# Performance work log

Measured on AMD Instinct MI355X. Metric: run time of the kernel, lower is better.

## Reference

```python
import jax, jax.numpy as jnp
import numpy as np

EPS = 1e-5
B, C, T = 128, 64, 1000          # batch, EEG channels, time samples
NCLU, HID, NOUT = 8, 512, 4      # clusters, head hidden dim, outputs (=feature_dim)


def _conv1d(x, w):
    # x: (N, Cin, T), w: (Cout, Cin, K), valid conv along time
    return jax.lax.conv_general_dilated(x, w, (1,), 'VALID',
                                        dimension_numbers=('NCH', 'OIH', 'NCH'))


def _bn(x, g, b, m, v):
    # eval-mode BatchNorm over channel dim of (N, C, T)
    return (x - m[None, :, None]) * (g / jnp.sqrt(v + EPS))[None, :, None] + b[None, :, None]


def _pool3(x):
    # maxpool kernel 3 stride 3 along time
    return jax.lax.reduce_window(x, -jnp.inf, jax.lax.max, (1, 1, 3), (1, 1, 3), 'VALID')


def setup_inputs() -> dict:
    key = jax.random.key(0)
    ks = jax.random.split(key, 12)
    def nrm(k, shape, fan):
        return jax.random.normal(k, shape, jnp.float32) / np.float32(np.sqrt(fan))
    inp = {
        'x': jax.random.normal(ks[0], (B, C, T), jnp.float32),
        'cluster_ids': jax.random.randint(ks[1], (B,), 0, NCLU, jnp.int32),
        # Deep4Net-style backbone params
        'w_time': nrm(ks[2], (25, 1, 10), 10),
        'b_time': jnp.zeros((25,), jnp.float32),
        'w_spat': nrm(ks[3], (25, 25, C), 25 * C),
        'w2': nrm(ks[4], (50, 25, 10), 250),
        'w3': nrm(ks[5], (100, 50, 10), 500),
        'w4': nrm(ks[6], (200, 100, 10), 1000),
        'w_cls': nrm(ks[7], (NOUT, 200, 7), 1400),
        'b_cls': jnp.zeros((NOUT,), jnp.float32),
        # per-cluster expert head params
        'hW1': nrm(ks[8], (NCLU, HID, NOUT), NOUT),
        'hb1': jnp.zeros((NCLU, HID), jnp.float32),
        'hW2': nrm(ks[9], (NCLU, NOUT, HID), HID),
        'hb2': jnp.zeros((NCLU, NOUT), jnp.float32),
        'hg': jnp.ones((NCLU, HID), jnp.float32),
        'hbe': jnp.zeros((NCLU, HID), jnp.float32),
        'hm': jnp.zeros((NCLU, HID), jnp.float32),
        'hv': jnp.ones((NCLU, HID), jnp.float32),
    }
    for i, c in zip((1, 2, 3, 4), (25, 50, 100, 200)):
        inp[f'g{i}'] = jnp.ones((c,), jnp.float32)
        inp[f'be{i}'] = jnp.zeros((c,), jnp.float32)
        inp[f'm{i}'] = jnp.zeros((c,), jnp.float32)
        inp[f'v{i}'] = jnp.ones((c,), jnp.float32)
    return inp


def reference(x, cluster_ids, w_time, b_time, w_spat, w2, w3, w4, w_cls, b_cls,
              hW1, hb1, hW2, hb2, hg, hbe, hm, hv,
              g1, be1, m1, v1, g2, be2, m2, v2, g3, be3, m3, v3, g4, be4, m4, v4):
    b_, c_, t_ = x.shape
    # conv_time: same 25 temporal filters applied per EEG channel -> (B, C, 25, T1)
    h = _conv1d(x.reshape(b_ * c_, 1, t_), w_time) + b_time[None, :, None]
    h = h.reshape(b_, c_, 25, -1)
    # conv_spat: collapse EEG channel axis -> (B, 25, T1)
    z = jnp.einsum('bcft,gfc->bgt', h, w_spat)
    z = _pool3(jax.nn.elu(_bn(z, g1, be1, m1, v1)))
    for w, g, be, m, v in ((w2, g2, be2, m2, v2), (w3, g3, be3, m3, v3), (w4, g4, be4, m4, v4)):
        z = _pool3(jax.nn.elu(_bn(_conv1d(z, w), g, be, m, v)))
    # final_conv_length='auto': classifier conv reduces time dim to 1 -> (B, NOUT)
    feats = (_conv1d(z, w_cls) + b_cls[None, :, None])[:, :, 0]
    # per-sample expert head routing (Linear -> BN(eval) -> ReLU -> [Dropout eval] -> Linear)
    h1 = jnp.einsum('bf,bhf->bh', feats, hW1[cluster_ids]) + hb1[cluster_ids]
    h1 = (h1 - hm[cluster_ids]) * (hg[cluster_ids] / jnp.sqrt(hv[cluster_ids] + EPS)) + hbe[cluster_ids]
    h1 = jax.nn.relu(h1)
    return jnp.einsum('bh,boh->bo', h1, hW2[cluster_ids]) + hb2[cluster_ids]
```

## Files before the change

### kernel.cpp

```cpp
#include <hip/hip_runtime.h>
#include <math.h>

#define EPS_BN 1e-5f

typedef __attribute__((ext_vector_type(8))) short short8;
typedef __attribute__((ext_vector_type(4))) float f32x4;
typedef __attribute__((ext_vector_type(4))) unsigned int uint4v;

__device__ __forceinline__ unsigned short f2bf(float f) {
    unsigned int u = __float_as_uint(f);
    u = (u + 0x7fffu + ((u >> 16) & 1u)) >> 16;
    return (unsigned short)u;
}
__device__ __forceinline__ float bf2f(unsigned short s) {
    return __uint_as_float(((unsigned int)s) << 16);
}
__device__ __forceinline__ float elu1(float y) { return y > 0.f ? y : expm1f(y); }
__device__ __forceinline__ float warp_sum(float v) {
    for (int off = 32; off > 0; off >>= 1) v += __shfl_down(v, off);
    return v;
}

#define UW1 0
#define UW2 20480
#define UW3 40960
#define UW4 122880
#define BB1 0
#define BB2 32
#define BB3 96
#define BB4 224
#define XTG_U 410496
#define Z1G_U 9192320
#define Z2G_U 10544000

#define NPREP 1602
#define RS_ZB 36

__global__ __launch_bounds__(256) void kprep_tr(
    const float* __restrict__ x,
    const float* __restrict__ w_time, const float* __restrict__ b_time,
    const float* __restrict__ w_spat,
    const float* __restrict__ w2, const float* __restrict__ w3,
    const float* __restrict__ w4,
    const float* __restrict__ g1, const float* __restrict__ be1,
    const float* __restrict__ m1, const float* __restrict__ v1,
    const float* __restrict__ g2, const float* __restrict__ be2,
    const float* __restrict__ m2, const float* __restrict__ v2,
    const float* __restrict__ g3, const float* __restrict__ be3,
    const float* __restrict__ m3, const float* __restrict__ v3,
    const float* __restrict__ g4, const float* __restrict__ be4,
    const float* __restrict__ m4, const float* __restrict__ v4,
    unsigned short* __restrict__ wsz, float* __restrict__ biasf) {
    __shared__ float tr[64 * 65];
    if (blockIdx.x < NPREP) {
        int idx = blockIdx.x * 256 + threadIdx.x;
        if (idx < 20480) {
            int k = idx >> 11, g = (idx >> 6) & 31, c = idx & 63;
            float val = 0.f;
            if (g < 25) {
                float s = 0.f;
#pragma unroll
                for (int f = 0; f < 25; ++f)
                    s = fmaf(w_spat[g * 1600 + f * 64 + c], w_time[f * 10 + k], s);
                val = s * (g1[g] * rsqrtf(v1[g] + EPS_BN));
            }
            wsz[UW1 + idx] = f2bf(val);
        } else if (idx < 40960) {
            int j = idx - 20480;
            int k = j >> 11, g = (j >> 5) & 63, c = j & 31;
            float val = 0.f;
            if (g < 50 && c < 25)
                val = w2[(g * 25 + c) * 10 + k] * (g2[g] * rsqrtf(v2[g] + EPS_BN));
            wsz[UW2 + j] = f2bf(val);
        } else if (idx < 122880) {
            int j = idx - 40960;
            int k = j >> 13, g = (j >> 6) & 127, c = j & 63;
            float val = 0.f;
            if (g < 100 && c < 50)
                val = w3[(g * 50 + c) * 10 + k] * (g3[g] * rsqrtf(v3[g] + EPS_BN));
            wsz[UW3 + j] = f2bf(val);
        } else if (idx < 409600) {
            int j = idx - 122880;
            int k = j / 28672, r = j % 28672, g = r >> 7, c = r & 127;
            float val = 0.f;
            if (g < 200 && c < 100)
                val = w4[(g * 100 + c) * 10 + k] * (g4[g] * rsqrtf(v4[g] + EPS_BN));
            wsz[UW4 + j] = f2bf(val);
        } else if (idx < 410048) {
            int j = idx - 409600;
            if (j < 32) {
                int g = j; float val = 0.f;
                if (g < 25) {
                    float beff = 0.f;
                    for (int f = 0; f < 25; ++f) {
                        float a = 0.f;
                        for (int c = 0; c < 64; ++c) a += w_spat[g * 1600 + f * 64 + c];
                        beff = fmaf(a, b_time[f], beff);
                    }
                    float sc = g1[g] * rsqrtf(v1[g] + EPS_BN);
                    val = be1[g] - m1[g] * sc + beff * sc;
                }
                biasf[BB1 + g] = val;
            } else if (j < 96) {
                int g = j - 32; float val = 0.f;
                if (g < 50) { float sc = g2[g] * rsqrtf(v2[g] + EPS_BN); val = be2[g] - m2[g] * sc; }
                biasf[BB2 + g] = val;
            } else if (j < 224) {
                int g = j - 96; float val = 0.f;
                if (g < 100) { float sc = g3[g] * rsqrtf(v3[g] + EPS_BN); val = be3[g] - m3[g] * sc; }
                biasf[BB3 + g] = val;
            } else {
                int g = j - 224; float val = 0.f;
                if (g < 200) { float sc = g4[g] * rsqrtf(v4[g] + EPS_BN); val = be4[g] - m4[g] * sc; }
                biasf[BB4 + g] = val;
            }
        }
    } else {
        const int bid = blockIdx.x - NPREP;
        const int b = bid / 17, tile = bid % 17, t = threadIdx.x;
        const int t0 = tile * 64;
        const float* xb = x + b * 64000;
        for (int idx = t; idx < 1024; idx += 256) {
            int c = idx >> 4, q = idx & 15;
            int tg = t0 + 4 * q;
            float4 v = {0.f, 0.f, 0.f, 0.f};
            if (tg + 4 <= 1000) {
                v = *(const float4*)(xb + c * 1000 + tg);
            } else {
                float* pv = (float*)&v;
#pragma unroll
                for (int e = 0; e < 4; ++e)
                    if (tg + e < 1000) pv[e] = xb[c * 1000 + tg + e];
            }
            tr[c * 65 + 4 * q]     = v.x;
            tr[c * 65 + 4 * q + 1] = v.y;
            tr[c * 65 + 4 * q + 2] = v.z;
            tr[c * 65 + 4 * q + 3] = v.w;
        }
        __syncthreads();
        unsigned short* xTg = wsz + XTG_U;
        for (int idx = t; idx < 2048; idx += 256) {
            int tl = idx >> 5, cp = idx & 31;
            int tg = t0 + tl;
            unsigned int pk = 0u;
            if (tg < 1000)
                pk = (unsigned int)f2bf(tr[(2 * cp) * 65 + tl]) |
                     ((unsigned int)f2bf(tr[(2 * cp + 1) * 65 + tl]) << 16);
            if (tg < 1072)
                *(unsigned int*)&xTg[(b * 1072 + tg) * 64 + 2 * cp] = pk;
        }
    }
}

template<int CPAD, int RS, int SP, int TT, int TPC, int NCHUNK, int JMAX,
         int NTCH, int GPAD, int TPOOL, int GSTORE, int NGV, int OUT_RS,
         bool OUT_F32, int NW>
__device__ __forceinline__ void conv_core(
    const unsigned short* xT, const unsigned short* __restrict__ wpk,
    const float* __restrict__ bias,
    unsigned short* zout, float* zoutf, unsigned short* zb,
    int t, int jbeg, int jend, int t0b) {
    const int lane = t & 63;
    const int wv = __builtin_amdgcn_readfirstlane(t >> 6);
    const int lm = lane & 15, h8 = lane >> 4;
    const int gloc = lane & 31, hh = lane >> 5;
    unsigned short* zbw = zb + wv * (48 * RS_ZB);

    for (int job = jbeg + wv; job < jend; job += NW) {
        const int gbi = job / NTCH, tci = job % NTCH;
        const int tl0 = tci * (TT * 16) - t0b;
        const int po0 = tci * (NCHUNK * 16);

        f32x4 acc[TT][2];
#pragma unroll
        for (int i = 0; i < TT; ++i) {
            acc[i][0] = (f32x4){0.f, 0.f, 0.f, 0.f};
            acc[i][1] = (f32x4){0.f, 0.f, 0.f, 0.f};
        }

        const int abase = (tl0 + lm) * RS + h8 * 8;
        const unsigned short* wp = wpk + (gbi * 32 + lm) * CPAD + h8 * 8;
#pragma unroll
        for (int k = 0; k < 10; ++k) {
            short8 w0[SP], w1[SP];
#pragma unroll
            for (int s = 0; s < SP; ++s) {
                w0[s] = *(const short8*)(wp + k * (GPAD * CPAD) + s * 32);
                w1[s] = *(const short8*)(wp + k * (GPAD * CPAD) + 16 * CPAD + s * 32);
            }
#pragma unroll
            for (int s = 0; s < SP; ++s) {
#pragma unroll
                for (int tt = 0; tt < TT; ++tt) {
                    short8 a = *(const short8*)&xT[abase + (tt * 16 + k) * RS + s * 32];
                    acc[tt][0] = __builtin_amdgcn_mfma_f32_16x16x32_bf16(
                        a, w0[s], acc[tt][0], 0, 0, 0);
                    acc[tt][1] = __builtin_amdgcn_mfma_f32_16x16x32_bf16(
                        a, w1[s], acc[tt][1], 0, 0, 0);
                }
            }
        }

        const float bv0 = bias[gbi * 32 + lm];
        const float bv1 = bias[gbi * 32 + 16 + lm];
#pragma unroll
        for (int ch = 0; ch < NCHUNK; ++ch) {
#pragma unroll
            for (int ti = 0; ti < TPC; ++ti) {
                int ttg = ch * TPC + ti;
#pragma unroll
                for (int r = 0; r < 4; ++r) {
                    float v0 = elu1(acc[ttg][0][r] + bv0);
                    float v1 = elu1(acc[ttg][1][r] + bv1);
                    int row = ti * 16 + 4 * h8 + r;
                    zbw[row * RS_ZB + lm] = f2bf(v0);
                    zbw[row * RS_ZB + 16 + lm] = f2bf(v1);
                }
            }
#pragma unroll
            for (int j = 0; j < JMAX; ++j) {
                int po = hh + 2 * j;
                if (3 * po + 2 < TPC * 16) {
                    float q0 = bf2f(zbw[(3 * po) * RS_ZB + gloc]);
                    float q1 = bf2f(zbw[(3 * po + 1) * RS_ZB + gloc]);
                    float q2 = bf2f(zbw[(3 * po + 2) * RS_ZB + gloc]);
                    float mx = fmaxf(q0, fmaxf(q1, q2));
                    int poa = po0 + ch * 16 + po;
                    int ga = gbi * 32 + gloc;
                    if (poa < TPOOL && ga < GSTORE) {
                        if constexpr (OUT_F32)
                            zoutf[poa * OUT_RS + ga] = mx;
                        else
                            zout[poa * OUT_RS + ga] =
                                (ga < NGV) ? f2bf(mx) : (unsigned short)0;
                    }
                }
            }
        }
    }
}

__global__ __launch_bounds__(64) void ks1(
    const unsigned short* __restrict__ wsu, const float* __restrict__ biasf,
    unsigned short* __restrict__ wsz) {
    __shared__ __align__(16) unsigned short xT[112 * 72];
    __shared__ __align__(16) unsigned short zb[48 * RS_ZB];
    const int b = blockIdx.x, tci = blockIdx.y, t = threadIdx.x;
    const int t0b = tci * 96;
    const unsigned short* xTg = wsz + XTG_U + (b * 1072 + t0b) * 64;
    for (int idx = t; idx < 112 * 8; idx += 64) {
        int r = idx >> 3, q = idx & 7;
        *(uint4v*)&xT[r * 72 + 8 * q] = *(const uint4v*)&xTg[r * 64 + 8 * q];
    }
    __syncthreads();
    conv_core<64, 72, 2, 6, 3, 2, 8, 11, 32, 330, 32, 25, 32, false, 1>(
        xT, wsu + UW1, biasf + BB1, wsz + Z1G_U + b * 330 * 32, nullptr, zb,
        t, tci, tci + 1, t0b);
}

__global__ __launch_bounds__(64) void ks2(
    const unsigned short* __restrict__ wsu, const float* __restrict__ biasf,
    unsigned short* __restrict__ wsz) {
    __shared__ __align__(16) unsigned short xT[112 * 40];
    __shared__ __align__(16) unsigned short zb[48 * RS_ZB];
    const int b = blockIdx.x, job = blockIdx.y, t = threadIdx.x;
    const int t0b = (job & 3) * 96;
    const unsigned short* z1g = wsz + Z1G_U + b * 330 * 32;
    for (int idx = t; idx < 112 * 4; idx += 64) {
        int r = idx >> 2, q = idx & 3;
        uint4v v = {0u, 0u, 0u, 0u};
        if (t0b + r < 330) v = *(const uint4v*)&z1g[(t0b + r) * 32 + 8 * q];
        *(uint4v*)&xT[r * 40 + 8 * q] = v;
    }
    __syncthreads();
    conv_core<32, 40, 1, 6, 3, 2, 8, 4, 64, 107, 64, 50, 64, false, 1>(
        xT, wsu + UW2, biasf + BB2, wsz + Z2G_U + b * 107 * 64, nullptr, zb,
        t, job, job + 1, t0b);
}

__global__ __launch_bounds__(256) void ks34h(
    const unsigned short* __restrict__ wsu, const float* __restrict__ biasf,
    unsigned short* __restrict__ wsz,
    const float* __restrict__ w_cls, const float* __restrict__ b_cls,
    const int* __restrict__ cid,
    const float* __restrict__ hW1, const float* __restrict__ hb1,
    const float* __restrict__ hW2, const float* __restrict__ hb2,
    const float* __restrict__ hg, const float* __restrict__ hbe,
    const float* __restrict__ hm, const float* __restrict__ hv,
    float* __restrict__ out) {
    __shared__ __align__(16) unsigned char smem[49600];
    unsigned short* z2t = (unsigned short*)(smem);
    unsigned short* z3t = (unsigned short*)(smem + 16128);
    float*          z4f = (float*)(smem + 28096);
    unsigned short* zb  = (unsigned short*)(smem + 33696);
    float*          feats = (float*)(smem + 47520);
    float*          h1s   = (float*)(smem + 47536);

    const int b = blockIdx.x, t = threadIdx.x;
    const unsigned short* z2g = wsz + Z2G_U + b * 107 * 64;
    for (int idx = t; idx < 112 * 8; idx += 256) {
        int r = idx >> 3, q = idx & 7;
        uint4v v = {0u, 0u, 0u, 0u};
        if (r < 107) v = *(const uint4v*)&z2g[r * 64 + 8 * q];
        *(uint4v*)&z2t[r * 72 + 8 * q] = v;
    }
    for (int i = t; i < 816; i += 256)
        *(unsigned int*)&z3t[32 * 136 + 2 * i] = 0u;
    __syncthreads();

    conv_core<64, 72, 2, 6, 3, 2, 8, 1, 128, 32, 128, 100, 136, false, 4>(
        z2t, wsu + UW3, biasf + BB3, z3t, nullptr, zb, t, 0, 4, 0);
    __syncthreads();

    conv_core<128, 136, 4, 2, 2, 1, 4, 1, 224, 7, 200, 200, 200, true, 4>(
        z3t, wsu + UW4, biasf + BB4, nullptr, z4f, zb, t, 0, 7, 0);
    __syncthreads();

    const int wv = t >> 6, lane = t & 63;
    {
        float p = 0.f;
        for (int i = lane; i < 1400; i += 64) {
            int po = i / 200, g = i - po * 200;
            p = fmaf(z4f[i], w_cls[wv * 1400 + g * 7 + po], p);
        }
        p = warp_sum(p);
        if (lane == 0) feats[wv] = p + b_cls[wv];
    }
    __syncthreads();

    const int c = cid[b];
    const float f0 = feats[0], f1 = feats[1], f2 = feats[2], f3 = feats[3];
    for (int h = t; h < 512; h += 256) {
        const float* w1 = &hW1[(c * 512 + h) * 4];
        float v = f0 * w1[0] + f1 * w1[1] + f2 * w1[2] + f3 * w1[3] + hb1[c * 512 + h];
        float sc = hg[c * 512 + h] * rsqrtf(hv[c * 512 + h] + EPS_BN);
        v = (v - hm[c * 512 + h]) * sc + hbe[c * 512 + h];
        h1s[h] = fmaxf(v, 0.f);
    }
    __syncthreads();
    {
        float p = 0.f;
        for (int i = lane; i < 512; i += 64)
            p = fmaf(h1s[i], hW2[(c * 4 + wv) * 512 + i], p);
        p = warp_sum(p);
        if (lane == 0) out[b * 4 + wv] = p + hb2[c * 4 + wv];
    }
}

extern "C" void kernel_launch(void* const* d_in, const int* in_sizes, int n_in,
                              void* d_out, int out_size, void* d_ws, size_t ws_size,
                              hipStream_t stream) {
    const float* x      = (const float*)d_in[0];
    const int*   cid    = (const int*)d_in[1];
    const float* w_time = (const float*)d_in[2];
    const float* b_time = (const float*)d_in[3];
    const float* w_spat = (const float*)d_in[4];
    const float* w2     = (const float*)d_in[5];
    const float* w3     = (const float*)d_in[6];
    const float* w4     = (const float*)d_in[7];
    const float* w_cls  = (const float*)d_in[8];
    const float* b_cls  = (const float*)d_in[9];
    const float* hW1    = (const float*)d_in[10];
    const float* hb1    = (const float*)d_in[11];
    const float* hW2    = (const float*)d_in[12];
    const float* hb2    = (const float*)d_in[13];
    const float* hg     = (const float*)d_in[14];
    const float* hbe    = (const float*)d_in[15];
    const float* hm     = (const float*)d_in[16];
    const float* hv     = (const float*)d_in[17];
    const float* g1  = (const float*)d_in[18];
    const float* be1 = (const float*)d_in[19];
    const float* m1  = (const float*)d_in[20];
    const float* v1  = (const float*)d_in[21];
    const float* g2  = (const float*)d_in[22];
    const float* be2 = (const float*)d_in[23];
    const float* m2  = (const float*)d_in[24];
    const float* v2  = (const float*)d_in[25];
    const float* g3  = (const float*)d_in[26];
    const float* be3 = (const float*)d_in[27];
    const float* m3  = (const float*)d_in[28];
    const float* v3  = (const float*)d_in[29];
    const float* g4  = (const float*)d_in[30];
    const float* be4 = (const float*)d_in[31];
    const float* m4  = (const float*)d_in[32];
    const float* v4  = (const float*)d_in[33];

    unsigned short* wsz = (unsigned short*)d_ws;
    float* biasf = (float*)((char*)d_ws + 819200);
    float* out = (float*)d_out;

    kprep_tr<<<NPREP + 128 * 17, 256, 0, stream>>>(
        x, w_time, b_time, w_spat, w2, w3, w4,
        g1, be1, m1, v1, g2, be2, m2, v2, g3, be3, m3, v3, g4, be4, m4, v4,
        wsz, biasf);

    ks1<<<dim3(128, 11), 64, 0, stream>>>(wsz, biasf, wsz);
    ks2<<<dim3(128, 8), 64, 0, stream>>>(wsz, biasf, wsz);
    ks34h<<<128, 256, 0, stream>>>(wsz, biasf, wsz, w_cls, b_cls, cid,
                                   hW1, hb1, hW2, hb2, hg, hbe, hm, hv, out);
}
```

Measured before the change: 108.0 us.

## Split fused conv3/conv4/head kernel into separate per-stage kernels with more blocks

```diff
diff --git a/kernel.cpp b/kernel.cpp
--- a/kernel.cpp
+++ b/kernel.cpp
@@ -32,6 +32,8 @@
 #define XTG_U 410496
 #define Z1G_U 9192320
 #define Z2G_U 10544000
+#define Z3G_U 11420544
+#define Z4G_BYTE 24372992
 
 #define NPREP 1602
 #define RS_ZB 36
@@ -278,9 +280,46 @@
         t, job, job + 1, t0b);
 }
 
-__global__ __launch_bounds__(256) void ks34h(
+__global__ __launch_bounds__(64) void ks3(
     const unsigned short* __restrict__ wsu, const float* __restrict__ biasf,
-    unsigned short* __restrict__ wsz,
+    unsigned short* __restrict__ wsz) {
+    __shared__ __align__(16) unsigned short z2t[112 * 72];
+    __shared__ __align__(16) unsigned short zb[48 * RS_ZB];
+    const int b = blockIdx.x, gbi = blockIdx.y, t = threadIdx.x;
+    const unsigned short* z2g = wsz + Z2G_U + b * 107 * 64;
+    for (int idx = t; idx < 112 * 8; idx += 64) {
+        int r = idx >> 3, q = idx & 7;
+        uint4v v = {0u, 0u, 0u, 0u};
+        if (r < 107) v = *(const uint4v*)&z2g[r * 64 + 8 * q];
+        *(uint4v*)&z2t[r * 72 + 8 * q] = v;
+    }
+    __syncthreads();
+    conv_core<64, 72, 2, 6, 3, 2, 8, 1, 128, 32, 128, 100, 136, false, 1>(
+        z2t, wsu + UW3, biasf + BB3, wsz + Z3G_U + b * 44 * 136, nullptr, zb,
+        t, gbi, gbi + 1, 0);
+}
+
+__global__ __launch_bounds__(64) void ks4(
+    const unsigned short* __restrict__ wsu, const float* __restrict__ biasf,
+    unsigned short* __restrict__ wsz, float* __restrict__ z4g) {
+    __shared__ __align__(16) unsigned short z3t[44 * 136];
+    __shared__ __align__(16) unsigned short zb[48 * RS_ZB];
+    const int b = blockIdx.x, gbi = blockIdx.y, t = threadIdx.x;
+    const unsigned short* z3g = wsz + Z3G_U + b * 44 * 136;
+    for (int idx = t; idx < 44 * 17; idx += 64) {
+        int r = idx / 17, q = idx % 17;
+        uint4v v = {0u, 0u, 0u, 0u};
+        if (r < 32) v = *(const uint4v*)&z3g[r * 136 + 8 * q];
+        *(uint4v*)&z3t[r * 136 + 8 * q] = v;
+    }
+    __syncthreads();
+    conv_core<128, 136, 4, 2, 2, 1, 4, 1, 224, 7, 200, 200, 200, true, 1>(
+        z3t, wsu + UW4, biasf + BB4, nullptr, z4g + b * 1400, zb,
+        t, gbi, gbi + 1, 0);
+}
+
+__global__ __launch_bounds__(256) void kh(
+    const float* __restrict__ z4g,
     const float* __restrict__ w_cls, const float* __restrict__ b_cls,
     const int* __restrict__ cid,
     const float* __restrict__ hW1, const float* __restrict__ hb1,
@@ -288,32 +327,11 @@
     const float* __restrict__ hg, const float* __restrict__ hbe,
     const float* __restrict__ hm, const float* __restrict__ hv,
     float* __restrict__ out) {
-    __shared__ __align__(16) unsigned char smem[49600];
-    unsigned short* z2t = (unsigned short*)(smem);
-    unsigned short* z3t = (unsigned short*)(smem + 16128);
-    float*          z4f = (float*)(smem + 28096);
-    unsigned short* zb  = (unsigned short*)(smem + 33696);
-    float*          feats = (float*)(smem + 47520);
-    float*          h1s   = (float*)(smem + 47536);
-
+    __shared__ float z4f[1400];
+    __shared__ float feats[4];
+    __shared__ float h1s[512];
     const int b = blockIdx.x, t = threadIdx.x;
-    const unsigned short* z2g = wsz + Z2G_U + b * 107 * 64;
-    for (int idx = t; idx < 112 * 8; idx += 256) {
-        int r = idx >> 3, q = idx & 7;
-        uint4v v = {0u, 0u, 0u, 0u};
-        if (r < 107) v = *(const uint4v*)&z2g[r * 64 + 8 * q];
-        *(uint4v*)&z2t[r * 72 + 8 * q] = v;
-    }
-    for (int i = t; i < 816; i += 256)
-        *(unsigned int*)&z3t[32 * 136 + 2 * i] = 0u;
-    __syncthreads();
-
-    conv_core<64, 72, 2, 6, 3, 2, 8, 1, 128, 32, 128, 100, 136, false, 4>(
-        z2t, wsu + UW3, biasf + BB3, z3t, nullptr, zb, t, 0, 4, 0);
-    __syncthreads();
-
-    conv_core<128, 136, 4, 2, 2, 1, 4, 1, 224, 7, 200, 200, 200, true, 4>(
-        z3t, wsu + UW4, biasf + BB4, nullptr, z4f, zb, t, 0, 7, 0);
+    for (int i = t; i < 1400; i += 256) z4f[i] = z4g[b * 1400 + i];
     __syncthreads();
 
     const int wv = t >> 6, lane = t & 63;
@@ -387,6 +405,7 @@
 
     unsigned short* wsz = (unsigned short*)d_ws;
     float* biasf = (float*)((char*)d_ws + 819200);
+    float* z4g   = (float*)((char*)d_ws + Z4G_BYTE);
     float* out = (float*)d_out;
 
     kprep_tr<<<NPREP + 128 * 17, 256, 0, stream>>>(
@@ -396,6 +415,8 @@
 
     ks1<<<dim3(128, 11), 64, 0, stream>>>(wsz, biasf, wsz);
     ks2<<<dim3(128, 8), 64, 0, stream>>>(wsz, biasf, wsz);
-    ks34h<<<128, 256, 0, stream>>>(wsz, biasf, wsz, w_cls, b_cls, cid,
-                                   hW1, hb1, hW2, hb2, hg, hbe, hm, hv, out);
-}
+    ks3<<<dim3(128, 4), 64, 0, stream>>>(wsz, biasf, wsz);
+    ks4<<<dim3(128, 7), 64, 0, stream>>>(wsz, biasf, wsz, z4g);
+    kh<<<128, 256, 0, stream>>>(z4g, w_cls, b_cls, cid, hW1, hb1, hW2, hb2,
+                                hg, hbe, hm, hv, out);
+}
```

Measured after the change: 109.0 us. No clear change (+0.9%).
